# Kernel tuning notes

Hardware: AMD Instinct MI355X
Metric: run time of the kernel (lower is better)

## Reference

```python
import jax, jax.numpy as jnp
from jax import lax
import numpy as np

B, T = 32, 15
THR1, THR2 = 15.0, 10.0  # conv1_t, conv2_t


def _conv(x, w):
    # x: (B,T,C,H,W) cumulative potentials/spikes; conv applied per timestep
    b, t, c, h, wd = x.shape
    y = lax.conv_general_dilated(x.reshape(b * t, c, h, wd), w, (1, 1), 'VALID',
                                 dimension_numbers=('NCHW', 'OIHW', 'NCHW'))
    return y.reshape(b, t, *y.shape[1:])


def _pool(x, k, s):
    b, t, c, h, wd = x.shape
    y = lax.reduce_window(x.reshape(b * t, c, h, wd), -jnp.inf, lax.max,
                          (1, 1, k, k), (1, 1, s, s), 'VALID')
    return y.reshape(b, t, *y.shape[1:])


def _pad(x, p):
    return jnp.pad(x, ((0, 0), (0, 0), (0, 0), (p, p), (p, p)))


def _fire(pot, thr):
    # sf.fire: F.threshold_(pot, thr, 0); spk = sign
    th = jnp.where(pot > thr, pot, 0.0)
    return jnp.sign(th), th


def _winner_class(pot, spk):
    # sf.get_k_winners(pot, kwta=1, r=0, spk): earliest spike, tie-break by potential
    b, t = spk.shape[:2]
    cnt = spk.sum(axis=1)                                   # (B,F,H,W) spike counts
    first = jnp.clip((t - cnt).astype(jnp.int32), 0, t - 1)  # earliest spike time
    vals = jnp.take_along_axis(pot, first[:, None], axis=1)[:, 0]  # pot at spike time
    trunc = spk * vals[:, None]                              # (B,T,F,H,W)
    v = trunc.reshape(b, -1).max(axis=1) * t                 # dominance offset per sample
    total = (trunc + spk * v[:, None, None, None, None]).sum(axis=1)  # (B,F,H,W)
    flat = total.reshape(b, -1)
    idx = jnp.argmax(flat, axis=1)
    mx = jnp.max(flat, axis=1)
    hw = pot.shape[-1] * pot.shape[-2]
    feat = idx // hw
    # decision_map: 10 classes x 20 features each -> class = feat // 20; -1 if no spike
    return jnp.where(mx != 0, feat // 20, -1).astype(jnp.int32)


def setup_inputs() -> dict:
    key = jax.random.key(0)
    k1, k2, k3, k4 = jax.random.split(key, 4)
    # cumulative binary spike wave: neuron fires at t_fire and stays 1 afterwards
    t_fire = jax.random.randint(k1, (B, 18, 32, 32), 0, T + 1)
    inp = (jnp.arange(T)[None, :, None, None, None] >= t_fire[:, None]).astype(jnp.float32)
    w1 = 0.8 + 0.05 * jax.random.normal(k2, (90, 18, 7, 7), dtype=jnp.float32)
    w2 = 0.8 + 0.05 * jax.random.normal(k3, (250, 90, 5, 5), dtype=jnp.float32)
    w3 = 0.8 + 0.05 * jax.random.normal(k4, (200, 250, 5, 5), dtype=jnp.float32)
    return {'input': inp, 'w1': w1, 'w2': w2, 'w3': w3, 'max_layer': 3}


def reference(input, w1, w2, w3, max_layer):
    # eval-mode forward of CIFAR10Net
    x = _pad(input, 2)                       # (B,T,18,36,36)
    spk1, pot1 = _fire(_conv(x, w1), THR1)   # (B,T,90,30,30)
    if max_layer == 1:
        return spk1, pot1
    spk2, pot2 = _fire(_conv(_pad(_pool(spk1, 2, 2), 1), w2), THR2)  # (B,T,250,13,13)
    if max_layer == 2:
        return spk2, pot2
    pot3 = _conv(_pad(_pool(spk2, 3, 3), 2), w3)   # (B,T,200,4,4)
    t = pot3.shape[1]
    mask = (jnp.arange(t) == t - 1).astype(pot3.dtype)[None, :, None, None, None]
    spk3 = jnp.sign(pot3 * mask)             # fire with threshold=None: only last step
    cls = _winner_class(pot3, spk3)          # (B,) predicted class or -1
    return cls, pot3
```

## Files before the change

kernel.cpp:

```cpp
#include <hip/hip_runtime.h>

#define NB 32
#define NT 15


__device__ __forceinline__ float gather8(const int* lst, int i, const char* wb) {
    int4 p0 = *(const int4*)(lst + i);
    int4 p1 = *(const int4*)(lst + i + 4);
    int o0 = __builtin_amdgcn_readfirstlane(p0.x);
    int o1 = __builtin_amdgcn_readfirstlane(p0.y);
    int o2 = __builtin_amdgcn_readfirstlane(p0.z);
    int o3 = __builtin_amdgcn_readfirstlane(p0.w);
    int o4 = __builtin_amdgcn_readfirstlane(p1.x);
    int o5 = __builtin_amdgcn_readfirstlane(p1.y);
    int o6 = __builtin_amdgcn_readfirstlane(p1.z);
    int o7 = __builtin_amdgcn_readfirstlane(p1.w);
    float a0 = *(const float*)(wb + o0);
    float a1 = *(const float*)(wb + o1);
    float a2 = *(const float*)(wb + o2);
    float a3 = *(const float*)(wb + o3);
    float a4 = *(const float*)(wb + o4);
    float a5 = *(const float*)(wb + o5);
    float a6 = *(const float*)(wb + o6);
    float a7 = *(const float*)(wb + o7);
    return ((a0 + a1) + (a2 + a3)) + ((a4 + a5) + (a6 + a7));
}

__device__ __forceinline__ void tr_tile(const float* __restrict__ src, float* __restrict__ dst,
                                        int F, int K, int KK, int CIN, int nkt, int t, int tid) {
    __shared__ float lds[32][33];
    int kt = t % nkt, ft = t / nkt;
    int k0 = kt * 32, f0 = ft * 32;
    int tx = tid & 31, ty = tid >> 5;
#pragma unroll
    for (int i = 0; i < 4; i++) {
        int fl = ty + 8 * i;
        int f = f0 + fl, k = k0 + tx;
        lds[fl][tx] = (f < F && k < K) ? src[(size_t)f * K + k] : 0.f;
    }
    __syncthreads();
#pragma unroll
    for (int i = 0; i < 4; i++) {
        int row = ty + 8 * i;
        int k = k0 + row, f = f0 + tx;
        if (k < K && f < F) {
            int j = (k % KK) * CIN + k / KK;
            dst[(size_t)j * F + f] = lds[tx][row];
        }
    }
}

__global__ __launch_bounds__(256) void k_pre(const float* __restrict__ inp,
                                             const float* __restrict__ w1,
                                             const float* __restrict__ w2,
                                             const float* __restrict__ w3,
                                             float* __restrict__ wT1, float* __restrict__ wT2,
                                             float* __restrict__ wT3,
                                             unsigned char* __restrict__ zmap,
                                             float* __restrict__ PosS2, float* __restrict__ PosS3,
                                             float* __restrict__ Pmin1,
                                             unsigned char* __restrict__ ft1,
                                             unsigned char* __restrict__ zmaps) {
    int blk = blockIdx.x, tid = threadIdx.x;
    if (blk < 2024) {
        const float* src; float* dst;
        int F, K, KK, CIN, nkt, t;
        if (blk < 84)       { src = w1; dst = wT1; F = 90;  K = 882;  KK = 49; CIN = 18;  nkt = 28;  t = blk; }
        else if (blk < 652) { src = w2; dst = wT2; F = 250; K = 2250; KK = 25; CIN = 90;  nkt = 71;  t = blk - 84; }
        else                { src = w3; dst = wT3; F = 200; K = 6250; KK = 25; CIN = 250; nkt = 196; t = blk - 652; }
        tr_tile(src, dst, F, K, KK, CIN, nkt, t, tid);
    } else if (blk == 2024) {
        if (tid < 90)  wT1[882 * 90 + tid] = 0.f;
        if (tid < 250) wT2[(size_t)2250 * 250 + tid] = 0.f;
        if (tid < 200) wT3[(size_t)6250 * 200 + tid] = 0.f;
    } else if (blk < 2187) {
        int idx = (blk - 2025) * 256 + tid;
        int xx = idx % 36, rest = idx / 36;
        int yy = rest % 36; int b = rest / 36;
        int z = 0;
        int x = xx - 2, y = yy - 2;
        if (x >= 0 && x < 32 && y >= 0 && y < 32) {
            const float* p = inp + (size_t)b * NT * 18 * 1024 + y * 32 + x;
#pragma unroll
            for (int c = 0; c < 18; c++) z += (p[(size_t)c * 1024] != 0.f);
        }
        zmap[idx] = (unsigned char)z;
    } else if (blk < 2212) {
        int idx = (blk - 2187) * 256 + tid;
        if (idx < 6250) {
            int f = idx / 25, pos = idx - f * 25;
            float acc = 0.f;
            for (int c = 0; c < 90; c++) acc += w2[(size_t)(f * 90 + c) * 25 + pos];
            PosS2[pos * 256 + f] = acc;
        }
    } else if (blk < 2232) {
        int idx = (blk - 2212) * 256 + tid;
        if (idx < 5000) {
            int f = idx / 25, pos = idx - f * 25;
            float acc = 0.f;
            for (int c = 0; c < 250; c++) acc += w3[(size_t)(f * 250 + c) * 25 + pos];
            PosS3[pos * 200 + f] = acc;
        }
    } else if (blk < 2272) {
        int bb = blk - 2232;
        __shared__ float wm[4];
        float m = 1e30f;
#pragma unroll
        for (int k = 0; k < 8; k++) {
            int i = bb * 2048 + k * 256 + tid;
            if (i < 90 * 882) m = fminf(m, w1[i]);
        }
        for (int o = 32; o > 0; o >>= 1) m = fminf(m, __shfl_down(m, o));
        if ((tid & 63) == 0) wm[tid >> 6] = m;
        __syncthreads();
        if (tid == 0) Pmin1[bb] = fminf(fminf(wm[0], wm[1]), fminf(wm[2], wm[3]));
    } else if (blk < 2905) {
        int i = (blk - 2272) * 256 + tid;
        if (i < 162000) ((uint4*)ft1)[i] = uint4{0, 0, 0, 0};
    } else {
        int i = (blk - 2905) * 256 + tid;
        if (i < 2150) ((uint4*)zmaps)[i] = uint4{0, 0, 0, 0};
    }
}

__global__ __launch_bounds__(256) void k_screen1(const unsigned char* __restrict__ zmap,
                                                 const float* __restrict__ Pmin1,
                                                 const float* __restrict__ PosS2,
                                                 const float* __restrict__ PosS3,
                                                 float* __restrict__ W2e, float* __restrict__ W3s,
                                                 int* __restrict__ cnt, int* __restrict__ list1) {
    int blk = blockIdx.x, tid = threadIdx.x;
    if (blk < 113) {
        int idx = blk * 256 + tid;
        if (idx < 28800) {
            int b = idx / 900, p = idx - b * 900;
            int oy = p / 30, ox = p - oy * 30;
            float m1 = 1e30f;
            for (int i = 0; i < 40; i++) m1 = fminf(m1, Pmin1[i]);
            int c0 = 0;
            const unsigned char* zb = zmap + (b * 36 + oy) * 36 + ox;
#pragma unroll
            for (int dy = 0; dy < 7; dy++)
#pragma unroll
                for (int dx = 0; dx < 7; dx++) c0 += zb[dy * 36 + dx];
            if (!((float)c0 * m1 > 15.0f)) {
                int pos = atomicAdd(cnt + 0, 1);
                list1[pos] = idx;
            }
        }
    } else if (blk < 282) {
        int p = blk - 113;
        int oy = p / 13, ox = p - oy * 13;
        int f = tid < 250 ? tid : 249;
        float W = 0.f;
#pragma unroll
        for (int pos = 0; pos < 25; pos++) {
            int r = pos / 5, x = pos - r * 5;
            int gy = oy + r, gx = ox + x;
            if (!(gy == 0 || gy == 16 || gx == 0 || gx == 16)) W += PosS2[pos * 256 + f];
        }
        if (tid < 250) W2e[p * 256 + tid] = W;
    } else {
        int i = (blk - 282) * 256 + tid;
        if (i < 3200) {
            int px = i / 200, f = i - px * 200;
            int oy = px >> 2, ox = px & 3;
            int r0 = max(0, 2 - oy), r1 = min(4, 5 - oy);
            int x0 = max(0, 2 - ox), x1 = min(4, 5 - ox);
            float s = 0.f;
            for (int r = r0; r <= r1; r++)
                for (int x = x0; x <= x1; x++) s += PosS3[(r * 5 + x) * 200 + f];
            W3s[px * 200 + f] = s;
        }
    }
}

__global__ __launch_bounds__(256) void k_hard1_fill(const float* __restrict__ inp,
                                                    const float* __restrict__ wT1,
                                                    const float* __restrict__ W2e,
                                                    const float* __restrict__ W3s,
                                                    const int* __restrict__ cnt,
                                                    const int* __restrict__ list1,
                                                    unsigned char* __restrict__ ft1,
                                                    unsigned char* __restrict__ nzc1,
                                                    unsigned char* __restrict__ ft2,
                                                    unsigned char* __restrict__ nz2any,
                                                    float* __restrict__ out) {
    __shared__ __align__(16) int slist[896];
    __shared__ int scnt, spcnt;
    int blk = blockIdx.x, tid = threadIdx.x;
    if (blk < 900) {
        int n = cnt[0];
        for (int it = blk; it < n; it += 900) {
            __syncthreads();
            int idx = list1[it];
            int b = idx / 900, p = idx - b * 900;
            int oy = p / 30, ox = p - oy * 30;
            unsigned char myft[4];
#pragma unroll
            for (int k = 0; k < 4; k++) {
                int j = tid + k * 256;
                unsigned char v = 255;
                if (j < 882) {
                    int dy = j / 126, rem = j - dy * 126;
                    int dx = rem / 18, c = rem - dx * 18;
                    int y = oy + dy - 2, x = ox + dx - 2;
                    v = 15;
                    if ((unsigned)y < 32u && (unsigned)x < 32u)
                        v = (inp[(size_t)b * 276480 + (size_t)c * 1024 + y * 32 + x] != 0.f) ? 0 : 200;
                }
                myft[k] = v;
            }
            int f = tid < 90 ? tid : 89;
            const char* wb = (const char*)(wT1 + f);
            const int zoff = 882 * 90 * 4;
            float acc = 0.f; int ftv = 15;
            for (int s = 0; s < 15; s++) {
                if (s == 1) {
#pragma unroll
                    for (int k = 0; k < 4; k++) {
                        if (myft[k] == 200) {
                            int j = tid + k * 256;
                            int dy = j / 126, rem = j - dy * 126;
                            int dx = rem / 18, c = rem - dx * 18;
                            int y = oy + dy - 2, x = ox + dx - 2;
                            const float* q = inp + (size_t)b * 276480 + (size_t)c * 1024 + y * 32 + x;
                            int cf = 0;
#pragma unroll
                            for (int t = 1; t < NT; t++) cf += (q[(size_t)t * 18432] != 0.f);
                            myft[k] = (unsigned char)(15 - cf);
                        }
                    }
                }
                if (tid == 0) scnt = 0;
                __syncthreads();
#pragma unroll
                for (int k = 0; k < 4; k++) {
                    if ((int)myft[k] == s) { int pp = atomicAdd(&scnt, 1); slist[pp] = (tid + k * 256) * 360; }
                }
                __syncthreads();
                if (tid == 0) {
                    int c0 = scnt, cp = (c0 + 7) & ~7;
                    for (int i = c0; i < cp; i++) slist[i] = zoff;
                    spcnt = cp;
                }
                __syncthreads();
                int e = spcnt;
                for (int i = 0; i < e; i += 8) acc += gather8(slist, i, wb);
                if (ftv == 15 && acc > 15.0f) ftv = s;
                if (__syncthreads_and(ftv != 15)) break;
            }
            if (tid < 90) {
                ft1[(size_t)idx * 90 + tid] = (unsigned char)ftv;
                if (ftv != 0) nzc1[idx] = 1;
            }
        }
    } else if (blk < 1231) {
        int i = (blk - 900) * 256 + tid;
        if (i < 84500) {
            union { unsigned char c[16]; uint4 v; } u;
            int g = i * 16;
#pragma unroll
            for (int k = 0; k < 16; k++) {
                int gg = g + k;
                int f = gg % 250;
                int p = (gg / 250) % 169;
                u.c[k] = (W2e[p * 256 + f] > 10.0f) ? 0 : 15;
            }
            *(uint4*)(ft2 + (size_t)g) = u.v;
        }
    } else if (blk == 1231) {
        if (tid < 169) {
            unsigned char any = 0;
            for (int f = 0; f < 250; f++) any |= (W2e[tid * 256 + f] <= 10.0f) ? 1 : 0;
            nz2any[tid] = any;
        }
    } else {
        int i = (blk - 1232) * 256 + tid;
        int g = i * 4;
        int px0 = g & 15;
        int f = (g >> 4) % 200;
        float4 v;
        v.x = W3s[(px0 + 0) * 200 + f];
        v.y = W3s[(px0 + 1) * 200 + f];
        v.z = W3s[(px0 + 2) * 200 + f];
        v.w = W3s[(px0 + 3) * 200 + f];
        *(float4*)(out + 32 + (size_t)g) = v;
    }
}

__global__ __launch_bounds__(256) void k_screen2(const unsigned char* __restrict__ nzc1,
                                                 const unsigned char* __restrict__ nz2any,
                                                 unsigned char* __restrict__ nzc2,
                                                 int* __restrict__ cnt, int* __restrict__ list2) {
    int idx = blockIdx.x * 256 + threadIdx.x;
    if (idx >= 5408) return;
    int b = idx / 169, p = idx - b * 169;
    int oy = p / 13, ox = p - oy * 13;
    int gy0 = max(1, oy), gy1 = min(15, oy + 4);
    int gx0 = max(1, ox), gx1 = min(15, ox + 4);
    int y0 = 2 * (gy0 - 1), y1 = 2 * (gy1 - 1) + 1;
    int x0 = 2 * (gx0 - 1), x1 = 2 * (gx1 - 1) + 1;
    int s = 0;
    const unsigned char* nb = nzc1 + b * 900;
    for (int y = y0; y <= y1; y++)
        for (int x = x0; x <= x1; x++) s += nb[y * 30 + x];
    nzc2[idx] = nz2any[p];
    if (s) { int pos = atomicAdd(cnt + 1, 1); list2[pos] = idx; }
}

__global__ __launch_bounds__(256) void k_hard2(const unsigned char* __restrict__ ft1,
                                               const float* __restrict__ wT2,
                                               const float* __restrict__ W2e,
                                               const int* __restrict__ cnt,
                                               const int* __restrict__ list2,
                                               unsigned char* __restrict__ ft2,
                                               unsigned char* __restrict__ nzc2) {
    constexpr int PADCAP = 2250 + 15 * 8;
    __shared__ __align__(16) int perm[PADCAP];
    __shared__ int start[16], cur[16];
    __shared__ int cntCs, anynz;
    int tid = threadIdx.x;
    int n = cnt[1];
    for (int it = blockIdx.x; it < n; it += 512) {
        __syncthreads();
        int idx = list2[it];
        int b = idx / 169, p = idx - b * 169;
        int oy = p / 13, ox = p - oy * 13;
        const unsigned char* fb = ft1 + (size_t)b * 81000;
        if (tid == 0) { cntCs = 0; anynz = 0; }
        if (tid < 16) cur[tid] = 0;
        unsigned char myft[9];
        int nc = 0;
#pragma unroll
        for (int k = 0; k < 9; k++) {
            int j = tid + k * 256;
            myft[k] = 0;
            if (j < 2250) {
                int r = j / 450, rem = j - r * 450;
                int x = rem / 90, c = rem - x * 90;
                int gy = oy + r, gx = ox + x;
                if (gy >= 1 && gy <= 15 && gx >= 1 && gx <= 15) {
                    const unsigned char* q = fb + ((size_t)((gy - 1) * 2) * 30 + (gx - 1) * 2) * 90 + c;
                    int m = q[0];
                    m = min(m, (int)q[90]);
                    m = min(m, (int)q[2700]);
                    m = min(m, (int)q[2790]);
                    myft[k] = (unsigned char)m;
                }
            }
            nc += (myft[k] >= 1);
        }
        for (int o = 32; o > 0; o >>= 1) nc += __shfl_down(nc, o);
        __syncthreads();
        if ((tid & 63) == 0) atomicAdd(&cntCs, nc);
        __syncthreads();
        int f = tid < 250 ? tid : 249;
        float W = W2e[p * 256 + f];
        int ftv;
        if (cntCs == 0) {
            ftv = (W > 10.0f) ? 0 : 15;
        } else {
#pragma unroll
            for (int k = 0; k < 9; k++) { int v = myft[k]; if (v >= 1) atomicAdd(&cur[v - 1], 1); }
            __syncthreads();
            if (tid == 0) {
                int s = 0;
#pragma unroll
                for (int j = 0; j < 15; j++) { int c = cur[j]; start[j] = s; s += (c + 7) & ~7; }
                start[15] = s;
            }
            __syncthreads();
            int nnzp = start[15];
            if (tid < 15) cur[tid] = start[tid];
            const int zoff = 2250 * 250 * 4;
            for (int i = tid; i < nnzp; i += 256) perm[i] = zoff;
            __syncthreads();
#pragma unroll
            for (int k = 0; k < 9; k++) {
                int v = myft[k];
                if (v >= 1) { int pp = atomicAdd(&cur[v - 1], 1); perm[pp] = (tid + k * 256) * 1000; }
            }
            __syncthreads();
            const char* wb = (const char*)(wT2 + f);
            float R = 0.f; int ft = 15;
            for (int j = 14; j >= 0; j--) {
                int sjb = start[j], e = start[j + 1];
                for (int i = sjb; i < e; i += 8) R += gather8(perm, i, wb);
                float pot = W - R;
                if (pot > 10.0f) ft = j;
                if (sjb == 0) { if (pot > 10.0f) ft = 0; break; }
                if (__all(pot <= 10.0f)) break;
            }
            ftv = ft;
        }
        if (tid < 250) {
            ft2[(size_t)idx * 250 + tid] = (unsigned char)ftv;
            if (ftv != 0) anynz = 1;
        }
        __syncthreads();
        if (tid == 0) nzc2[idx] = (unsigned char)(anynz ? 1 : 0);
    }
}

__global__ __launch_bounds__(256) void k_screen3(const unsigned char* __restrict__ nzc2,
                                                 int* __restrict__ cnt, int* __restrict__ list3) {
    int idx = blockIdx.x * 256 + threadIdx.x;
    if (idx >= 512) return;
    int b = idx >> 4, p = idx & 15;
    int oy = p >> 2, ox = p & 3;
    int r0 = max(0, 2 - oy), r1 = min(4, 5 - oy);
    int x0 = max(0, 2 - ox), x1 = min(4, 5 - ox);
    int py0 = oy + r0 - 2, py1 = oy + r1 - 2;
    int qx0 = ox + x0 - 2, qx1 = ox + x1 - 2;
    int s = 0;
    const unsigned char* nb = nzc2 + b * 169;
    for (int y = 3 * py0; y <= 3 * py1 + 2; y++)
        for (int x = 3 * qx0; x <= 3 * qx1 + 2; x++) s += nb[y * 13 + x];
    if (s) { int pos = atomicAdd(cnt + 2, 1); list3[pos] = idx; }
}

__global__ __launch_bounds__(256) void k_hard3(const unsigned char* __restrict__ ft2,
                                               const float* __restrict__ wT3,
                                               const float* __restrict__ W3s,
                                               const int* __restrict__ cnt,
                                               const int* __restrict__ list3,
                                               float* __restrict__ out) {
    constexpr int PADCAP = 4000 + 15 * 8;
    __shared__ __align__(16) int perm[PADCAP];
    __shared__ int start[16], cur[16];
    __shared__ int fbs[16], rowb[16];
    int tid = threadIdx.x;
    int n = cnt[2];
    for (int it = blockIdx.x; it < n; it += 256) {
        __syncthreads();
        int idx = list3[it];
        int b = idx >> 4, p = idx & 15;
        int oy = p >> 2, ox = p & 3;
        int r0 = max(0, 2 - oy), r1 = min(4, 5 - oy);
        int x0 = max(0, 2 - ox), x1 = min(4, 5 - ox);
        int VR = r1 - r0 + 1, VC = x1 - x0 + 1;
        int NP = VR * VC, NV = NP * 250;
        const unsigned char* fb = ft2 + (size_t)b * 42250;
        if (tid < NP) {
            int rv = tid / VC, xv = tid - rv * VC;
            int py = oy + r0 + rv - 2, pxx = ox + x0 + xv - 2;
            fbs[tid]  = (py * 3 * 13 + pxx * 3) * 250;
            rowb[tid] = ((r0 + rv) * 5 + (x0 + xv)) * 250;
        }
        if (tid < 16) cur[tid] = 0;
        __syncthreads();
        unsigned char myft[16];
#pragma unroll
        for (int k = 0; k < 16; k++) {
            int i = tid + k * 256;
            myft[k] = 0;
            if (i < NV) {
                int posv = i / 250, c = i - posv * 250;
                const unsigned char* q = fb + fbs[posv] + c;
                int m = q[0];
#pragma unroll
                for (int dy = 0; dy < 3; dy++)
#pragma unroll
                    for (int dx = 0; dx < 3; dx++)
                        if (dy | dx) m = min(m, (int)q[(dy * 13 + dx) * 250]);
                myft[k] = (unsigned char)m;
            }
        }
#pragma unroll
        for (int k = 0; k < 16; k++) { int v = myft[k]; if (v >= 1) atomicAdd(&cur[v - 1], 1); }
        __syncthreads();
        if (tid == 0) {
            int s = 0;
#pragma unroll
            for (int j = 0; j < 15; j++) { int c = cur[j]; start[j] = s; s += (c + 7) & ~7; }
            start[15] = s;
        }
        __syncthreads();
        int nnzp = start[15];
        if (tid < 15) cur[tid] = start[tid];
        const int zoff = 6250 * 200 * 4;
        for (int i = tid; i < nnzp; i += 256) perm[i] = zoff;
        __syncthreads();
#pragma unroll
        for (int k = 0; k < 16; k++) {
            int v = myft[k];
            if (v >= 1) {
                int i = tid + k * 256;
                int posv = i / 250, c = i - posv * 250;
                int pp = atomicAdd(&cur[v - 1], 1);
                perm[pp] = (rowb[posv] + c) * 800;
            }
        }
        __syncthreads();

        int f = tid < 200 ? tid : 199;
        const char* wb = (const char*)(wT3 + f);
        float W = W3s[p * 200 + f];
        float* o = out + 32 + ((size_t)b * NT) * 3200 + f * 16 + p;
        float R = 0.f;
        for (int j = 14; j >= 0; j--) {
            int sjb = start[j], e = start[j + 1];
            for (int i = sjb; i < e; i += 8) R += gather8(perm, i, wb);
            float pot = W - R;
            if (tid < 200) o[(size_t)j * 3200] = pot;
            if (sjb == 0) {
                for (int jj = j - 1; jj >= 0; jj--)
                    if (tid < 200) o[(size_t)jj * 3200] = pot;
                break;
            }
        }
    }
}

__global__ __launch_bounds__(256) void k_winner(const float* __restrict__ outp,
                                                float* __restrict__ outc) {
    int b = blockIdx.x, tid = threadIdx.x;
    const float* p14 = outp + 32 + ((size_t)b * NT + 14) * 3200;
    __shared__ float sv[256];
    __shared__ int   si[256];
    float m = 0.f;
    for (int j = tid; j < 3200; j += 256) {
        float v = p14[j];
        if (v > 0.f && v > m) m = v;
    }
    sv[tid] = m;
    __syncthreads();
    for (int s = 128; s > 0; s >>= 1) {
        if (tid < s) sv[tid] = fmaxf(sv[tid], sv[tid + s]);
        __syncthreads();
    }
    float vofs = 15.f * sv[0];
    __syncthreads();
    float bestv = 0.f; int besti = 0x3fffffff;
    for (int j = tid; j < 3200; j += 256) {
        float v = p14[j];
        float tot = (v > 0.f) ? v + vofs : 0.f;
        if (tot > bestv) { bestv = tot; besti = j; }
    }
    sv[tid] = bestv; si[tid] = besti;
    __syncthreads();
    for (int s = 128; s > 0; s >>= 1) {
        if (tid < s) {
            if (sv[tid + s] > sv[tid] || (sv[tid + s] == sv[tid] && si[tid + s] < si[tid])) {
                sv[tid] = sv[tid + s]; si[tid] = si[tid + s];
            }
        }
        __syncthreads();
    }
    if (tid == 0) {
        float mx = sv[0];
        int cls = (mx != 0.f) ? ((si[0] / 16) / 20) : -1;
        outc[b] = (float)cls;
    }
}

extern "C" void kernel_launch(void* const* d_in, const int* in_sizes, int n_in,
                              void* d_out, int out_size, void* d_ws, size_t ws_size,
                              hipStream_t stream) {
    const float* inp = (const float*)d_in[0];
    const float* w1  = (const float*)d_in[1];
    const float* w2  = (const float*)d_in[2];
    const float* w3  = (const float*)d_in[3];
    float* out = (float*)d_out;

    unsigned char* ws   = (unsigned char*)d_ws;
    unsigned char* ft1  = ws + 0;
    unsigned char* ft2  = ws + 2592000;
    float* wT1   = (float*)(ws + 3944000);
    float* wT2   = (float*)(ws + 4261888);
    float* wT3   = (float*)(ws + 6512896);
    float* PosS2 = (float*)(ws + 11513728);
    float* PosS3 = (float*)(ws + 11539328);
    float* W2e   = (float*)(ws + 11559328);
    float* W3s   = (float*)(ws + 11732384);
    float* Pmin1 = (float*)(ws + 11745184);
    unsigned char* zmap   = ws + 11745440;
    unsigned char* nzc1   = ws + 11786912;
    unsigned char* nzc2   = ws + 11815712;
    unsigned char* nz2any = ws + 11821120;
    int* cnt    = (int*)(ws + 11821296);
    int* list1  = (int*)(ws + 11821312);
    int* list2  = (int*)(ws + 11936512);
    int* list3  = (int*)(ws + 11958144);

    hipLaunchKernelGGL(k_pre, dim3(2914), dim3(256), 0, stream,
                       inp, w1, w2, w3, wT1, wT2, wT3, zmap, PosS2, PosS3, Pmin1, ft1, nzc1);
    hipLaunchKernelGGL(k_screen1, dim3(295), dim3(256), 0, stream,
                       zmap, Pmin1, PosS2, PosS3, W2e, W3s, cnt, list1);
    hipLaunchKernelGGL(k_hard1_fill, dim3(2732), dim3(256), 0, stream,
                       inp, wT1, W2e, W3s, cnt, list1, ft1, nzc1, ft2, nz2any, out);
    hipLaunchKernelGGL(k_screen2, dim3(22), dim3(256), 0, stream, nzc1, nz2any, nzc2, cnt, list2);
    hipLaunchKernelGGL(k_hard2, dim3(512), dim3(256), 0, stream, ft1, wT2, W2e, cnt, list2, ft2, nzc2);
    hipLaunchKernelGGL(k_screen3, dim3(2), dim3(256), 0, stream, nzc2, cnt, list3);
    hipLaunchKernelGGL(k_hard3, dim3(256), dim3(256), 0, stream, ft2, wT3, W3s, cnt, list3, out);
    hipLaunchKernelGGL(k_winner, dim3(NB), dim3(256), 0, stream, out, out);
}
```

Baseline: 155.8 us.

## Fold screening passes into conv kernels with per-block early exit

```diff
diff --git a/kernel.cpp b/kernel.cpp
--- a/kernel.cpp
+++ b/kernel.cpp
@@ -60,7 +60,7 @@
                                              float* __restrict__ PosS2, float* __restrict__ PosS3,
                                              float* __restrict__ Pmin1,
                                              unsigned char* __restrict__ ft1,
-                                             unsigned char* __restrict__ zmaps) {
+                                             unsigned char* __restrict__ nzc1) {
     int blk = blockIdx.x, tid = threadIdx.x;
     if (blk < 2024) {
         const float* src; float* dst;
@@ -119,37 +119,101 @@
         if (i < 162000) ((uint4*)ft1)[i] = uint4{0, 0, 0, 0};
     } else {
         int i = (blk - 2905) * 256 + tid;
-        if (i < 2150) ((uint4*)zmaps)[i] = uint4{0, 0, 0, 0};
-    }
-}
-
-__global__ __launch_bounds__(256) void k_screen1(const unsigned char* __restrict__ zmap,
-                                                 const float* __restrict__ Pmin1,
-                                                 const float* __restrict__ PosS2,
-                                                 const float* __restrict__ PosS3,
-                                                 float* __restrict__ W2e, float* __restrict__ W3s,
-                                                 int* __restrict__ cnt, int* __restrict__ list1) {
+        if (i < 1800) ((uint4*)nzc1)[i] = uint4{0, 0, 0, 0};
+    }
+}
+
+__global__ __launch_bounds__(256) void k_conv1(const float* __restrict__ inp,
+                                               const unsigned char* __restrict__ zmap,
+                                               const float* __restrict__ Pmin1,
+                                               const float* __restrict__ wT1,
+                                               const float* __restrict__ PosS2,
+                                               const float* __restrict__ PosS3,
+                                               unsigned char* __restrict__ ft1,
+                                               unsigned char* __restrict__ nzc1,
+                                               float* __restrict__ W2e,
+                                               unsigned char* __restrict__ ft2,
+                                               unsigned char* __restrict__ nzc2,
+                                               float* __restrict__ W3s) {
+    __shared__ __align__(16) int slist[896];
+    __shared__ int scnt, spcnt, cnt0s;
+    __shared__ float sm1;
     int blk = blockIdx.x, tid = threadIdx.x;
-    if (blk < 113) {
-        int idx = blk * 256 + tid;
-        if (idx < 28800) {
-            int b = idx / 900, p = idx - b * 900;
-            int oy = p / 30, ox = p - oy * 30;
-            float m1 = 1e30f;
-            for (int i = 0; i < 40; i++) m1 = fminf(m1, Pmin1[i]);
-            int c0 = 0;
-            const unsigned char* zb = zmap + (b * 36 + oy) * 36 + ox;
-#pragma unroll
-            for (int dy = 0; dy < 7; dy++)
-#pragma unroll
-                for (int dx = 0; dx < 7; dx++) c0 += zb[dy * 36 + dx];
-            if (!((float)c0 * m1 > 15.0f)) {
-                int pos = atomicAdd(cnt + 0, 1);
-                list1[pos] = idx;
-            }
-        }
-    } else if (blk < 282) {
-        int p = blk - 113;
+    if (blk < 28800) {
+        int b = blk / 900, p = blk - b * 900;
+        int oy = p / 30, ox = p - oy * 30;
+        int zv = 0;
+        if (tid < 49) zv = zmap[(b * 36 + oy + tid / 7) * 36 + ox + tid % 7];
+        float mm = (tid < 40) ? Pmin1[tid] : 1e30f;
+        if (tid < 64) {
+            for (int o = 32; o > 0; o >>= 1) {
+                zv += __shfl_down(zv, o);
+                mm = fminf(mm, __shfl_down(mm, o));
+            }
+            if (tid == 0) { cnt0s = zv; sm1 = mm; }
+        }
+        __syncthreads();
+        if ((float)cnt0s * sm1 > 15.0f) return;
+        unsigned char myft[4];
+#pragma unroll
+        for (int k = 0; k < 4; k++) {
+            int j = tid + k * 256;
+            unsigned char v = 255;
+            if (j < 882) {
+                int dy = j / 126, rem = j - dy * 126;
+                int dx = rem / 18, c = rem - dx * 18;
+                int y = oy + dy - 2, x = ox + dx - 2;
+                v = 15;
+                if ((unsigned)y < 32u && (unsigned)x < 32u)
+                    v = (inp[(size_t)b * 276480 + (size_t)c * 1024 + y * 32 + x] != 0.f) ? 0 : 200;
+            }
+            myft[k] = v;
+        }
+        int f = tid < 90 ? tid : 89;
+        const char* wb = (const char*)(wT1 + f);
+        const int zoff = 882 * 90 * 4;
+        float acc = 0.f; int ftv = 15;
+        for (int s = 0; s < 15; s++) {
+            if (s == 1) {
+#pragma unroll
+                for (int k = 0; k < 4; k++) {
+                    if (myft[k] == 200) {
+                        int j = tid + k * 256;
+                        int dy = j / 126, rem = j - dy * 126;
+                        int dx = rem / 18, c = rem - dx * 18;
+                        int y = oy + dy - 2, x = ox + dx - 2;
+                        const float* q = inp + (size_t)b * 276480 + (size_t)c * 1024 + y * 32 + x;
+                        int cf = 0;
+#pragma unroll
+                        for (int t = 1; t < NT; t++) cf += (q[(size_t)t * 18432] != 0.f);
+                        myft[k] = (unsigned char)(15 - cf);
+                    }
+                }
+            }
+            if (tid == 0) scnt = 0;
+            __syncthreads();
+#pragma unroll
+            for (int k = 0; k < 4; k++) {
+                if ((int)myft[k] == s) { int pp = atomicAdd(&scnt, 1); slist[pp] = (tid + k * 256) * 360; }
+            }
+            __syncthreads();
+            if (tid == 0) {
+                int c0 = scnt, cp = (c0 + 7) & ~7;
+                for (int i = c0; i < cp; i++) slist[i] = zoff;
+                spcnt = cp;
+            }
+            __syncthreads();
+            int e = spcnt;
+            for (int i = 0; i < e; i += 8) acc += gather8(slist, i, wb);
+            if (ftv == 15 && acc > 15.0f) ftv = s;
+            if (__syncthreads_and(ftv != 15)) break;
+        }
+        if (tid < 90) {
+            ft1[(size_t)blk * 90 + tid] = (unsigned char)ftv;
+            if (ftv != 0) nzc1[blk] = 1;
+        }
+    } else if (blk < 28969) {
+        int p = blk - 28800;
         int oy = p / 13, ox = p - oy * 13;
         int f = tid < 250 ? tid : 249;
         float W = 0.f;
@@ -160,123 +224,40 @@
             if (!(gy == 0 || gy == 16 || gx == 0 || gx == 16)) W += PosS2[pos * 256 + f];
         }
         if (tid < 250) W2e[p * 256 + tid] = W;
+        unsigned char v = (W > 10.0f) ? 0 : 15;
+        if (tid < 250)
+            for (int b = 0; b < NB; b++) ft2[(size_t)(b * 169 + p) * 250 + tid] = v;
+        int nz = (tid < 250 && W <= 10.0f) ? 1 : 0;
+        int any = __syncthreads_or(nz);
+        if (tid < NB) nzc2[tid * 169 + p] = (unsigned char)any;
     } else {
-        int i = (blk - 282) * 256 + tid;
-        if (i < 3200) {
-            int px = i / 200, f = i - px * 200;
-            int oy = px >> 2, ox = px & 3;
-            int r0 = max(0, 2 - oy), r1 = min(4, 5 - oy);
-            int x0 = max(0, 2 - ox), x1 = min(4, 5 - ox);
-            float s = 0.f;
-            for (int r = r0; r <= r1; r++)
-                for (int x = x0; x <= x1; x++) s += PosS3[(r * 5 + x) * 200 + f];
-            W3s[px * 200 + f] = s;
-        }
-    }
-}
-
-__global__ __launch_bounds__(256) void k_hard1_fill(const float* __restrict__ inp,
-                                                    const float* __restrict__ wT1,
-                                                    const float* __restrict__ W2e,
-                                                    const float* __restrict__ W3s,
-                                                    const int* __restrict__ cnt,
-                                                    const int* __restrict__ list1,
-                                                    unsigned char* __restrict__ ft1,
-                                                    unsigned char* __restrict__ nzc1,
-                                                    unsigned char* __restrict__ ft2,
-                                                    unsigned char* __restrict__ nz2any,
-                                                    float* __restrict__ out) {
-    __shared__ __align__(16) int slist[896];
-    __shared__ int scnt, spcnt;
+        int px = blk - 28969;
+        int f = tid < 200 ? tid : 199;
+        int oy = px >> 2, ox = px & 3;
+        int r0 = max(0, 2 - oy), r1 = min(4, 5 - oy);
+        int x0 = max(0, 2 - ox), x1 = min(4, 5 - ox);
+        float s = 0.f;
+        for (int r = r0; r <= r1; r++)
+            for (int x = x0; x <= x1; x++) s += PosS3[(r * 5 + x) * 200 + f];
+        if (tid < 200) W3s[px * 200 + tid] = s;
+    }
+}
+
+__global__ __launch_bounds__(256) void k_conv2(const unsigned char* __restrict__ ft1,
+                                               const unsigned char* __restrict__ nzc1,
+                                               const float* __restrict__ wT2,
+                                               const float* __restrict__ W2e,
+                                               const float* __restrict__ W3s,
+                                               unsigned char* __restrict__ ft2,
+                                               unsigned char* __restrict__ nzc2,
+                                               float* __restrict__ out) {
+    constexpr int PADCAP = 2250 + 15 * 8;
+    __shared__ __align__(16) int perm[PADCAP];
+    __shared__ int start[16], cur[16];
+    __shared__ int cntCs, anynz;
     int blk = blockIdx.x, tid = threadIdx.x;
-    if (blk < 900) {
-        int n = cnt[0];
-        for (int it = blk; it < n; it += 900) {
-            __syncthreads();
-            int idx = list1[it];
-            int b = idx / 900, p = idx - b * 900;
-            int oy = p / 30, ox = p - oy * 30;
-            unsigned char myft[4];
-#pragma unroll
-            for (int k = 0; k < 4; k++) {
-                int j = tid + k * 256;
-                unsigned char v = 255;
-                if (j < 882) {
-                    int dy = j / 126, rem = j - dy * 126;
-                    int dx = rem / 18, c = rem - dx * 18;
-                    int y = oy + dy - 2, x = ox + dx - 2;
-                    v = 15;
-                    if ((unsigned)y < 32u && (unsigned)x < 32u)
-                        v = (inp[(size_t)b * 276480 + (size_t)c * 1024 + y * 32 + x] != 0.f) ? 0 : 200;
-                }
-                myft[k] = v;
-            }
-            int f = tid < 90 ? tid : 89;
-            const char* wb = (const char*)(wT1 + f);
-            const int zoff = 882 * 90 * 4;
-            float acc = 0.f; int ftv = 15;
-            for (int s = 0; s < 15; s++) {
-                if (s == 1) {
-#pragma unroll
-                    for (int k = 0; k < 4; k++) {
-                        if (myft[k] == 200) {
-                            int j = tid + k * 256;
-                            int dy = j / 126, rem = j - dy * 126;
-                            int dx = rem / 18, c = rem - dx * 18;
-                            int y = oy + dy - 2, x = ox + dx - 2;
-                            const float* q = inp + (size_t)b * 276480 + (size_t)c * 1024 + y * 32 + x;
-                            int cf = 0;
-#pragma unroll
-                            for (int t = 1; t < NT; t++) cf += (q[(size_t)t * 18432] != 0.f);
-                            myft[k] = (unsigned char)(15 - cf);
-                        }
-                    }
-                }
-                if (tid == 0) scnt = 0;
-                __syncthreads();
-#pragma unroll
-                for (int k = 0; k < 4; k++) {
-                    if ((int)myft[k] == s) { int pp = atomicAdd(&scnt, 1); slist[pp] = (tid + k * 256) * 360; }
-                }
-                __syncthreads();
-                if (tid == 0) {
-                    int c0 = scnt, cp = (c0 + 7) & ~7;
-                    for (int i = c0; i < cp; i++) slist[i] = zoff;
-                    spcnt = cp;
-                }
-                __syncthreads();
-                int e = spcnt;
-                for (int i = 0; i < e; i += 8) acc += gather8(slist, i, wb);
-                if (ftv == 15 && acc > 15.0f) ftv = s;
-                if (__syncthreads_and(ftv != 15)) break;
-            }
-            if (tid < 90) {
-                ft1[(size_t)idx * 90 + tid] = (unsigned char)ftv;
-                if (ftv != 0) nzc1[idx] = 1;
-            }
-        }
-    } else if (blk < 1231) {
-        int i = (blk - 900) * 256 + tid;
-        if (i < 84500) {
-            union { unsigned char c[16]; uint4 v; } u;
-            int g = i * 16;
-#pragma unroll
-            for (int k = 0; k < 16; k++) {
-                int gg = g + k;
-                int f = gg % 250;
-                int p = (gg / 250) % 169;
-                u.c[k] = (W2e[p * 256 + f] > 10.0f) ? 0 : 15;
-            }
-            *(uint4*)(ft2 + (size_t)g) = u.v;
-        }
-    } else if (blk == 1231) {
-        if (tid < 169) {
-            unsigned char any = 0;
-            for (int f = 0; f < 250; f++) any |= (W2e[tid * 256 + f] <= 10.0f) ? 1 : 0;
-            nz2any[tid] = any;
-        }
-    } else {
-        int i = (blk - 1232) * 256 + tid;
+    if (blk >= 5408) {
+        int i = (blk - 5408) * 256 + tid;
         int g = i * 4;
         int px0 = g & 15;
         int f = (g >> 4) % 200;
@@ -286,229 +267,190 @@
         v.z = W3s[(px0 + 2) * 200 + f];
         v.w = W3s[(px0 + 3) * 200 + f];
         *(float4*)(out + 32 + (size_t)g) = v;
-    }
-}
-
-__global__ __launch_bounds__(256) void k_screen2(const unsigned char* __restrict__ nzc1,
-                                                 const unsigned char* __restrict__ nz2any,
-                                                 unsigned char* __restrict__ nzc2,
-                                                 int* __restrict__ cnt, int* __restrict__ list2) {
-    int idx = blockIdx.x * 256 + threadIdx.x;
-    if (idx >= 5408) return;
+        return;
+    }
+    int idx = blk;
     int b = idx / 169, p = idx - b * 169;
     int oy = p / 13, ox = p - oy * 13;
     int gy0 = max(1, oy), gy1 = min(15, oy + 4);
     int gx0 = max(1, ox), gx1 = min(15, ox + 4);
     int y0 = 2 * (gy0 - 1), y1 = 2 * (gy1 - 1) + 1;
     int x0 = 2 * (gx0 - 1), x1 = 2 * (gx1 - 1) + 1;
-    int s = 0;
+    int Wd = x1 - x0 + 1, cells = (y1 - y0 + 1) * Wd;
     const unsigned char* nb = nzc1 + b * 900;
-    for (int y = y0; y <= y1; y++)
-        for (int x = x0; x <= x1; x++) s += nb[y * 30 + x];
-    nzc2[idx] = nz2any[p];
-    if (s) { int pos = atomicAdd(cnt + 1, 1); list2[pos] = idx; }
-}
-
-__global__ __launch_bounds__(256) void k_hard2(const unsigned char* __restrict__ ft1,
-                                               const float* __restrict__ wT2,
-                                               const float* __restrict__ W2e,
-                                               const int* __restrict__ cnt,
-                                               const int* __restrict__ list2,
-                                               unsigned char* __restrict__ ft2,
-                                               unsigned char* __restrict__ nzc2) {
-    constexpr int PADCAP = 2250 + 15 * 8;
+    int v = 0;
+    if (tid < cells) { int yy = y0 + tid / Wd, xx = x0 + tid % Wd; v = nb[yy * 30 + xx]; }
+    int dirty = __syncthreads_or(v);
+    if (!dirty) return;
+    const unsigned char* fb = ft1 + (size_t)b * 81000;
+    if (tid == 0) { cntCs = 0; anynz = 0; }
+    if (tid < 16) cur[tid] = 0;
+    unsigned char myft[9];
+    int nc = 0;
+#pragma unroll
+    for (int k = 0; k < 9; k++) {
+        int j = tid + k * 256;
+        myft[k] = 0;
+        if (j < 2250) {
+            int r = j / 450, rem = j - r * 450;
+            int x = rem / 90, c = rem - x * 90;
+            int gy = oy + r, gx = ox + x;
+            if (gy >= 1 && gy <= 15 && gx >= 1 && gx <= 15) {
+                const unsigned char* q = fb + ((size_t)((gy - 1) * 2) * 30 + (gx - 1) * 2) * 90 + c;
+                int m = q[0];
+                m = min(m, (int)q[90]);
+                m = min(m, (int)q[2700]);
+                m = min(m, (int)q[2790]);
+                myft[k] = (unsigned char)m;
+            }
+        }
+        nc += (myft[k] >= 1);
+    }
+    for (int o = 32; o > 0; o >>= 1) nc += __shfl_down(nc, o);
+    __syncthreads();
+    if ((tid & 63) == 0) atomicAdd(&cntCs, nc);
+    __syncthreads();
+    int f = tid < 250 ? tid : 249;
+    float W = W2e[p * 256 + f];
+    int ftv;
+    if (cntCs == 0) {
+        ftv = (W > 10.0f) ? 0 : 15;
+    } else {
+#pragma unroll
+        for (int k = 0; k < 9; k++) { int vv = myft[k]; if (vv >= 1) atomicAdd(&cur[vv - 1], 1); }
+        __syncthreads();
+        if (tid == 0) {
+            int s = 0;
+#pragma unroll
+            for (int j = 0; j < 15; j++) { int c = cur[j]; start[j] = s; s += (c + 7) & ~7; }
+            start[15] = s;
+        }
+        __syncthreads();
+        int nnzp = start[15];
+        if (tid < 15) cur[tid] = start[tid];
+        const int zoff = 2250 * 250 * 4;
+        for (int i = tid; i < nnzp; i += 256) perm[i] = zoff;
+        __syncthreads();
+#pragma unroll
+        for (int k = 0; k < 9; k++) {
+            int vv = myft[k];
+            if (vv >= 1) { int pp = atomicAdd(&cur[vv - 1], 1); perm[pp] = (tid + k * 256) * 1000; }
+        }
+        __syncthreads();
+        const char* wb = (const char*)(wT2 + f);
+        float R = 0.f; int ft = 15;
+        for (int j = 14; j >= 0; j--) {
+            int sjb = start[j], e = start[j + 1];
+            for (int i = sjb; i < e; i += 8) R += gather8(perm, i, wb);
+            float pot = W - R;
+            if (pot > 10.0f) ft = j;
+            if (sjb == 0) { if (pot > 10.0f) ft = 0; break; }
+            if (__all(pot <= 10.0f)) break;
+        }
+        ftv = ft;
+    }
+    if (tid < 250) {
+        ft2[(size_t)idx * 250 + tid] = (unsigned char)ftv;
+        if (ftv != 0) anynz = 1;
+    }
+    __syncthreads();
+    if (tid == 0) nzc2[idx] = (unsigned char)(anynz ? 1 : 0);
+}
+
+__global__ __launch_bounds__(256) void k_conv3(const unsigned char* __restrict__ ft2,
+                                               const unsigned char* __restrict__ nzc2,
+                                               const float* __restrict__ wT3,
+                                               const float* __restrict__ W3s,
+                                               float* __restrict__ out) {
+    constexpr int PADCAP = 4000 + 15 * 8;
     __shared__ __align__(16) int perm[PADCAP];
     __shared__ int start[16], cur[16];
-    __shared__ int cntCs, anynz;
-    int tid = threadIdx.x;
-    int n = cnt[1];
-    for (int it = blockIdx.x; it < n; it += 512) {
-        __syncthreads();
-        int idx = list2[it];
-        int b = idx / 169, p = idx - b * 169;
-        int oy = p / 13, ox = p - oy * 13;
-        const unsigned char* fb = ft1 + (size_t)b * 81000;
-        if (tid == 0) { cntCs = 0; anynz = 0; }
-        if (tid < 16) cur[tid] = 0;
-        unsigned char myft[9];
-        int nc = 0;
-#pragma unroll
-        for (int k = 0; k < 9; k++) {
-            int j = tid + k * 256;
-            myft[k] = 0;
-            if (j < 2250) {
-                int r = j / 450, rem = j - r * 450;
-                int x = rem / 90, c = rem - x * 90;
-                int gy = oy + r, gx = ox + x;
-                if (gy >= 1 && gy <= 15 && gx >= 1 && gx <= 15) {
-                    const unsigned char* q = fb + ((size_t)((gy - 1) * 2) * 30 + (gx - 1) * 2) * 90 + c;
-                    int m = q[0];
-                    m = min(m, (int)q[90]);
-                    m = min(m, (int)q[2700]);
-                    m = min(m, (int)q[2790]);
-                    myft[k] = (unsigned char)m;
-                }
-            }
-            nc += (myft[k] >= 1);
-        }
-        for (int o = 32; o > 0; o >>= 1) nc += __shfl_down(nc, o);
-        __syncthreads();
-        if ((tid & 63) == 0) atomicAdd(&cntCs, nc);
-        __syncthreads();
-        int f = tid < 250 ? tid : 249;
-        float W = W2e[p * 256 + f];
-        int ftv;
-        if (cntCs == 0) {
-            ftv = (W > 10.0f) ? 0 : 15;
-        } else {
-#pragma unroll
-            for (int k = 0; k < 9; k++) { int v = myft[k]; if (v >= 1) atomicAdd(&cur[v - 1], 1); }
-            __syncthreads();
-            if (tid == 0) {
-                int s = 0;
-#pragma unroll
-                for (int j = 0; j < 15; j++) { int c = cur[j]; start[j] = s; s += (c + 7) & ~7; }
-                start[15] = s;
-            }
-            __syncthreads();
-            int nnzp = start[15];
-            if (tid < 15) cur[tid] = start[tid];
-            const int zoff = 2250 * 250 * 4;
-            for (int i = tid; i < nnzp; i += 256) perm[i] = zoff;
-            __syncthreads();
-#pragma unroll
-            for (int k = 0; k < 9; k++) {
-                int v = myft[k];
-                if (v >= 1) { int pp = atomicAdd(&cur[v - 1], 1); perm[pp] = (tid + k * 256) * 1000; }
-            }
-            __syncthreads();
-            const char* wb = (const char*)(wT2 + f);
-            float R = 0.f; int ft = 15;
-            for (int j = 14; j >= 0; j--) {
-                int sjb = start[j], e = start[j + 1];
-                for (int i = sjb; i < e; i += 8) R += gather8(perm, i, wb);
-                float pot = W - R;
-                if (pot > 10.0f) ft = j;
-                if (sjb == 0) { if (pot > 10.0f) ft = 0; break; }
-                if (__all(pot <= 10.0f)) break;
-            }
-            ftv = ft;
-        }
-        if (tid < 250) {
-            ft2[(size_t)idx * 250 + tid] = (unsigned char)ftv;
-            if (ftv != 0) anynz = 1;
-        }
-        __syncthreads();
-        if (tid == 0) nzc2[idx] = (unsigned char)(anynz ? 1 : 0);
-    }
-}
-
-__global__ __launch_bounds__(256) void k_screen3(const unsigned char* __restrict__ nzc2,
-                                                 int* __restrict__ cnt, int* __restrict__ list3) {
-    int idx = blockIdx.x * 256 + threadIdx.x;
-    if (idx >= 512) return;
+    __shared__ int fbs[16], rowb[16];
+    int blk = blockIdx.x, tid = threadIdx.x;
+    int idx = blk;
     int b = idx >> 4, p = idx & 15;
     int oy = p >> 2, ox = p & 3;
     int r0 = max(0, 2 - oy), r1 = min(4, 5 - oy);
     int x0 = max(0, 2 - ox), x1 = min(4, 5 - ox);
     int py0 = oy + r0 - 2, py1 = oy + r1 - 2;
     int qx0 = ox + x0 - 2, qx1 = ox + x1 - 2;
-    int s = 0;
-    const unsigned char* nb = nzc2 + b * 169;
-    for (int y = 3 * py0; y <= 3 * py1 + 2; y++)
-        for (int x = 3 * qx0; x <= 3 * qx1 + 2; x++) s += nb[y * 13 + x];
-    if (s) { int pos = atomicAdd(cnt + 2, 1); list3[pos] = idx; }
-}
-
-__global__ __launch_bounds__(256) void k_hard3(const unsigned char* __restrict__ ft2,
-                                               const float* __restrict__ wT3,
-                                               const float* __restrict__ W3s,
-                                               const int* __restrict__ cnt,
-                                               const int* __restrict__ list3,
-                                               float* __restrict__ out) {
-    constexpr int PADCAP = 4000 + 15 * 8;
-    __shared__ __align__(16) int perm[PADCAP];
-    __shared__ int start[16], cur[16];
-    __shared__ int fbs[16], rowb[16];
-    int tid = threadIdx.x;
-    int n = cnt[2];
-    for (int it = blockIdx.x; it < n; it += 256) {
-        __syncthreads();
-        int idx = list3[it];
-        int b = idx >> 4, p = idx & 15;
-        int oy = p >> 2, ox = p & 3;
-        int r0 = max(0, 2 - oy), r1 = min(4, 5 - oy);
-        int x0 = max(0, 2 - ox), x1 = min(4, 5 - ox);
-        int VR = r1 - r0 + 1, VC = x1 - x0 + 1;
-        int NP = VR * VC, NV = NP * 250;
-        const unsigned char* fb = ft2 + (size_t)b * 42250;
-        if (tid < NP) {
-            int rv = tid / VC, xv = tid - rv * VC;
-            int py = oy + r0 + rv - 2, pxx = ox + x0 + xv - 2;
-            fbs[tid]  = (py * 3 * 13 + pxx * 3) * 250;
-            rowb[tid] = ((r0 + rv) * 5 + (x0 + xv)) * 250;
-        }
-        if (tid < 16) cur[tid] = 0;
-        __syncthreads();
-        unsigned char myft[16];
-#pragma unroll
-        for (int k = 0; k < 16; k++) {
+    int sy0 = 3 * py0, sy1 = 3 * py1 + 2;
+    int sx0 = 3 * qx0, sx1 = 3 * qx1 + 2;
+    int Wd = sx1 - sx0 + 1, cells = (sy1 - sy0 + 1) * Wd;
+    const unsigned char* nb2 = nzc2 + b * 169;
+    int v = 0;
+    if (tid < cells) { int yy = sy0 + tid / Wd, xx = sx0 + tid % Wd; v = nb2[yy * 13 + xx]; }
+    int dirty = __syncthreads_or(v);
+    if (!dirty) return;
+    int VR = r1 - r0 + 1, VC = x1 - x0 + 1;
+    int NP = VR * VC, NV = NP * 250;
+    const unsigned char* fb = ft2 + (size_t)b * 42250;
+    if (tid < NP) {
+        int rv = tid / VC, xv = tid - rv * VC;
+        int py = oy + r0 + rv - 2, pxx = ox + x0 + xv - 2;
+        fbs[tid]  = (py * 3 * 13 + pxx * 3) * 250;
+        rowb[tid] = ((r0 + rv) * 5 + (x0 + xv)) * 250;
+    }
+    if (tid < 16) cur[tid] = 0;
+    __syncthreads();
+    unsigned char myft[16];
+#pragma unroll
+    for (int k = 0; k < 16; k++) {
+        int i = tid + k * 256;
+        myft[k] = 0;
+        if (i < NV) {
+            int posv = i / 250, c = i - posv * 250;
+            const unsigned char* q = fb + fbs[posv] + c;
+            int m = q[0];
+#pragma unroll
+            for (int dy = 0; dy < 3; dy++)
+#pragma unroll
+                for (int dx = 0; dx < 3; dx++)
+                    if (dy | dx) m = min(m, (int)q[(dy * 13 + dx) * 250]);
+            myft[k] = (unsigned char)m;
+        }
+    }
+#pragma unroll
+    for (int k = 0; k < 16; k++) { int vv = myft[k]; if (vv >= 1) atomicAdd(&cur[vv - 1], 1); }
+    __syncthreads();
+    if (tid == 0) {
+        int s = 0;
+#pragma unroll
+        for (int j = 0; j < 15; j++) { int c = cur[j]; start[j] = s; s += (c + 7) & ~7; }
+        start[15] = s;
+    }
+    __syncthreads();
+    int nnzp = start[15];
+    if (tid < 15) cur[tid] = start[tid];
+    const int zoff = 6250 * 200 * 4;
+    for (int i = tid; i < nnzp; i += 256) perm[i] = zoff;
+    __syncthreads();
+#pragma unroll
+    for (int k = 0; k < 16; k++) {
+        int vv = myft[k];
+        if (vv >= 1) {
             int i = tid + k * 256;
-            myft[k] = 0;
-            if (i < NV) {
-                int posv = i / 250, c = i - posv * 250;
-                const unsigned char* q = fb + fbs[posv] + c;
-                int m = q[0];
-#pragma unroll
-                for (int dy = 0; dy < 3; dy++)
-#pragma unroll
-                    for (int dx = 0; dx < 3; dx++)
-                        if (dy | dx) m = min(m, (int)q[(dy * 13 + dx) * 250]);
-                myft[k] = (unsigned char)m;
-            }
-        }
-#pragma unroll
-        for (int k = 0; k < 16; k++) { int v = myft[k]; if (v >= 1) atomicAdd(&cur[v - 1], 1); }
-        __syncthreads();
-        if (tid == 0) {
-            int s = 0;
-#pragma unroll
-            for (int j = 0; j < 15; j++) { int c = cur[j]; start[j] = s; s += (c + 7) & ~7; }
-            start[15] = s;
-        }
-        __syncthreads();
-        int nnzp = start[15];
-        if (tid < 15) cur[tid] = start[tid];
-        const int zoff = 6250 * 200 * 4;
-        for (int i = tid; i < nnzp; i += 256) perm[i] = zoff;
-        __syncthreads();
-#pragma unroll
-        for (int k = 0; k < 16; k++) {
-            int v = myft[k];
-            if (v >= 1) {
-                int i = tid + k * 256;
-                int posv = i / 250, c = i - posv * 250;
-                int pp = atomicAdd(&cur[v - 1], 1);
-                perm[pp] = (rowb[posv] + c) * 800;
-            }
-        }
-        __syncthreads();
-
-        int f = tid < 200 ? tid : 199;
-        const char* wb = (const char*)(wT3 + f);
-        float W = W3s[p * 200 + f];
-        float* o = out + 32 + ((size_t)b * NT) * 3200 + f * 16 + p;
-        float R = 0.f;
-        for (int j = 14; j >= 0; j--) {
-            int sjb = start[j], e = start[j + 1];
-            for (int i = sjb; i < e; i += 8) R += gather8(perm, i, wb);
-            float pot = W - R;
-            if (tid < 200) o[(size_t)j * 3200] = pot;
-            if (sjb == 0) {
-                for (int jj = j - 1; jj >= 0; jj--)
-                    if (tid < 200) o[(size_t)jj * 3200] = pot;
-                break;
-            }
+            int posv = i / 250, c = i - posv * 250;
+            int pp = atomicAdd(&cur[vv - 1], 1);
+            perm[pp] = (rowb[posv] + c) * 800;
+        }
+    }
+    __syncthreads();
+
+    int f = tid < 200 ? tid : 199;
+    const char* wb = (const char*)(wT3 + f);
+    float W = W3s[p * 200 + f];
+    float* o = out + 32 + ((size_t)b * NT) * 3200 + f * 16 + p;
+    float R = 0.f;
+    for (int j = 14; j >= 0; j--) {
+        int sjb = start[j], e = start[j + 1];
+        for (int i = sjb; i < e; i += 8) R += gather8(perm, i, wb);
+        float pot = W - R;
+        if (tid < 200) o[(size_t)j * 3200] = pot;
+        if (sjb == 0) {
+            for (int jj = j - 1; jj >= 0; jj--)
+                if (tid < 200) o[(size_t)jj * 3200] = pot;
+            break;
         }
     }
 }
@@ -575,24 +517,16 @@
     float* W2e   = (float*)(ws + 11559328);
     float* W3s   = (float*)(ws + 11732384);
     float* Pmin1 = (float*)(ws + 11745184);
-    unsigned char* zmap   = ws + 11745440;
-    unsigned char* nzc1   = ws + 11786912;
-    unsigned char* nzc2   = ws + 11815712;
-    unsigned char* nz2any = ws + 11821120;
-    int* cnt    = (int*)(ws + 11821296);
-    int* list1  = (int*)(ws + 11821312);
-    int* list2  = (int*)(ws + 11936512);
-    int* list3  = (int*)(ws + 11958144);
-
-    hipLaunchKernelGGL(k_pre, dim3(2914), dim3(256), 0, stream,
+    unsigned char* zmap = ws + 11745440;
+    unsigned char* nzc1 = ws + 11786912;
+    unsigned char* nzc2 = ws + 11815712;
+
+    hipLaunchKernelGGL(k_pre, dim3(2913), dim3(256), 0, stream,
                        inp, w1, w2, w3, wT1, wT2, wT3, zmap, PosS2, PosS3, Pmin1, ft1, nzc1);
-    hipLaunchKernelGGL(k_screen1, dim3(295), dim3(256), 0, stream,
-                       zmap, Pmin1, PosS2, PosS3, W2e, W3s, cnt, list1);
-    hipLaunchKernelGGL(k_hard1_fill, dim3(2732), dim3(256), 0, stream,
-                       inp, wT1, W2e, W3s, cnt, list1, ft1, nzc1, ft2, nz2any, out);
-    hipLaunchKernelGGL(k_screen2, dim3(22), dim3(256), 0, stream, nzc1, nz2any, nzc2, cnt, list2);
-    hipLaunchKernelGGL(k_hard2, dim3(512), dim3(256), 0, stream, ft1, wT2, W2e, cnt, list2, ft2, nzc2);
-    hipLaunchKernelGGL(k_screen3, dim3(2), dim3(256), 0, stream, nzc2, cnt, list3);
-    hipLaunchKernelGGL(k_hard3, dim3(256), dim3(256), 0, stream, ft2, wT3, W3s, cnt, list3, out);
+    hipLaunchKernelGGL(k_conv1, dim3(28985), dim3(256), 0, stream,
+                       inp, zmap, Pmin1, wT1, PosS2, PosS3, ft1, nzc1, W2e, ft2, nzc2, W3s);
+    hipLaunchKernelGGL(k_conv2, dim3(6908), dim3(256), 0, stream,
+                       ft1, nzc1, wT2, W2e, W3s, ft2, nzc2, out);
+    hipLaunchKernelGGL(k_conv3, dim3(512), dim3(256), 0, stream, ft2, nzc2, wT3, W3s, out);
     hipLaunchKernelGGL(k_winner, dim3(NB), dim3(256), 0, stream, out, out);
 }
```

Result: no change. 156.9 us (+0.7%).
